# Performance work log

Measured on AMD Instinct MI355X. Metric: run time of the kernel, lower is better.

## Reference

```python
import jax, jax.numpy as jnp
import numpy as np

N = 100000
NUM_CLASSES = 10
EPS = 1e-16
NEG_SLOPE = 0.2


def gat_conv(x, src, dst, W, a_src, a_dst, bias, heads, out_ch, concat):
    # x: [N, F_in]; src/dst: [E] (message flows src -> dst, PyG convention)
    n = x.shape[0]
    h = (x @ W).reshape(n, heads, out_ch)              # [N, H, C]
    al = jnp.sum(h * a_src, axis=-1)                   # [N, H] source attention term
    ar = jnp.sum(h * a_dst, axis=-1)                   # [N, H] target attention term
    e = jax.nn.leaky_relu(al[src] + ar[dst], NEG_SLOPE)  # [E, H]
    # segment softmax over incoming edges of each dst node
    m = jax.ops.segment_max(e, dst, num_segments=n)    # [N, H]
    ex = jnp.exp(e - m[dst])                           # [E, H]
    denom = jax.ops.segment_sum(ex, dst, num_segments=n)  # [N, H]
    alpha = ex / (denom[dst] + EPS)                    # [E, H]
    msg = h[src] * alpha[..., None]                    # [E, H, C]
    out = jax.ops.segment_sum(msg, dst, num_segments=n)   # [N, H, C]
    out = out.reshape(n, heads * out_ch) if concat else out.mean(axis=1)
    return out + bias


def setup_inputs() -> dict:
    key = jax.random.key(0)
    ks = jax.random.split(key, 10)
    F_in, H1, C1 = 512, 8, 8
    x = jax.random.normal(ks[0], (N, F_in), dtype=jnp.float32)
    edge_index = jax.random.randint(ks[1], (2, 1600000), 0, N, dtype=jnp.int64)
    s = 0.05
    return {
        "x": x,
        "edge_index": edge_index,
        "W1": jax.random.normal(ks[2], (F_in, H1 * C1), dtype=jnp.float32) * s,
        "a_src1": jax.random.normal(ks[3], (H1, C1), dtype=jnp.float32) * s,
        "a_dst1": jax.random.normal(ks[4], (H1, C1), dtype=jnp.float32) * s,
        "b1": jnp.zeros((H1 * C1,), dtype=jnp.float32),
        "W2": jax.random.normal(ks[5], (H1 * C1, NUM_CLASSES), dtype=jnp.float32) * s,
        "a_src2": jax.random.normal(ks[6], (1, NUM_CLASSES), dtype=jnp.float32) * s,
        "a_dst2": jax.random.normal(ks[7], (1, NUM_CLASSES), dtype=jnp.float32) * s,
        "b2": jnp.zeros((NUM_CLASSES,), dtype=jnp.float32),
    }


def reference(x, edge_index, W1, a_src1, a_dst1, b1, W2, a_src2, a_dst2, b2):
    # add self-loops (GATConv default add_self_loops=True)
    loops = jnp.arange(N, dtype=edge_index.dtype)
    src = jnp.concatenate([edge_index[0], loops])
    dst = jnp.concatenate([edge_index[1], loops])
    # eval mode: dropout(p=0.6) is identity
    h = gat_conv(x, src, dst, W1, a_src1, a_dst1, b1, heads=8, out_ch=8, concat=True)
    h = jax.nn.elu(h)
    out = gat_conv(h, src, dst, W2, a_src2, a_dst2, b2, heads=1, out_ch=NUM_CLASSES, concat=True)
    return jax.nn.log_softmax(out, axis=1)
```

## Files before the change

kernel.cpp:

```cpp
#include <hip/hip_runtime.h>
#include <math.h>

#define NN 100000
#define NEDGE 1600000
#define NTOT 1700000
#define FIN 512
#define NH1 8
#define NC1 8
#define F1 64
#define NC2 10
#define SLOPE 0.2f
#define EPSF 1e-16f
#define SCAN_BLK 1024
#define NB ((NN + SCAN_BLK - 1) / SCAN_BLK)

__device__ __forceinline__ float lrelu(float x) { return x > 0.f ? x : SLOPE * x; }
__device__ __forceinline__ float eluf(float x) { return x > 0.f ? x : __expf(x) - 1.f; }

__device__ __forceinline__ unsigned short f2bf_rne(float f) {
    unsigned int u = __float_as_uint(f);
    unsigned int r = (u + 0x7FFFu + ((u >> 16) & 1u)) >> 16;
    return (unsigned short)r;
}
__device__ __forceinline__ float bf2f(unsigned short b) {
    return __uint_as_float(((unsigned int)b) << 16);
}

#define GBM 256
#define GBK 32
#define AS_STRIDE 260

__global__ __launch_bounds__(256) void k_gemm1(const float* __restrict__ x,
                                               const float* __restrict__ W,
                                               const float* __restrict__ asrc,
                                               const float* __restrict__ adst,
                                               unsigned short* __restrict__ h1b,
                                               float* __restrict__ al,
                                               float* __restrict__ ar)
{
    __shared__ float As[GBK][AS_STRIDE];
    __shared__ float Bs[GBK][F1];
    __shared__ float sas[F1], sad[F1];
    const int tid = threadIdx.x;
    const int row0 = blockIdx.x * GBM;
    const int ti = tid >> 3;
    const int tj = tid & 7;
    const int ti8 = ti << 3, tj8 = tj << 3;
    if (tid < F1) { sas[tid] = asrc[tid]; sad[tid] = adst[tid]; }
    float acc[8][8] = {};

    for (int k0 = 0; k0 < FIN; k0 += GBK) {
        #pragma unroll
        for (int l = 0; l < 8; ++l) {
            int idx = tid + l * 256;
            int r = idx >> 3, c4 = idx & 7;
            int gr = row0 + r;
            float4 v = make_float4(0.f, 0.f, 0.f, 0.f);
            if (gr < NN) v = *(const float4*)(x + (size_t)gr * FIN + k0 + (c4 << 2));
            As[(c4 << 2) + 0][r] = v.x;
            As[(c4 << 2) + 1][r] = v.y;
            As[(c4 << 2) + 2][r] = v.z;
            As[(c4 << 2) + 3][r] = v.w;
        }
        #pragma unroll
        for (int l = 0; l < 2; ++l) {
            int idx = tid + l * 256;
            int r = idx >> 4, c4 = idx & 15;
            *(float4*)&Bs[r][c4 << 2] = *(const float4*)(W + (size_t)(k0 + r) * F1 + (c4 << 2));
        }
        __syncthreads();
        #pragma unroll
        for (int kk = 0; kk < GBK; ++kk) {
            float4 a0 = *(const float4*)&As[kk][ti8];
            float4 a1 = *(const float4*)&As[kk][ti8 + 4];
            float4 b0 = *(const float4*)&Bs[kk][tj8];
            float4 b1 = *(const float4*)&Bs[kk][tj8 + 4];
            float a[8] = {a0.x, a0.y, a0.z, a0.w, a1.x, a1.y, a1.z, a1.w};
            float b[8] = {b0.x, b0.y, b0.z, b0.w, b1.x, b1.y, b1.z, b1.w};
            #pragma unroll
            for (int i = 0; i < 8; ++i)
                #pragma unroll
                for (int j = 0; j < 8; ++j)
                    acc[i][j] += a[i] * b[j];
        }
        __syncthreads();
    }
    #pragma unroll
    for (int i = 0; i < 8; ++i) {
        int gr = row0 + ti8 + i;
        if (gr >= NN) break;
        float av = 0.f, dv = 0.f;
        unsigned short u[8];
        #pragma unroll
        for (int c = 0; c < 8; ++c) {
            av += acc[i][c] * sas[tj8 + c];
            dv += acc[i][c] * sad[tj8 + c];
            u[c] = f2bf_rne(acc[i][c]);
        }
        al[gr * NH1 + tj] = av;
        ar[gr * NH1 + tj] = dv;
        *(uint4*)(h1b + (size_t)gr * F1 + tj8) = *(uint4*)u;
    }
}

__global__ void k_init1(int* __restrict__ cnt)
{
    int i = blockIdx.x * blockDim.x + threadIdx.x;
    if (i < NN) cnt[i] = 1;
}

__global__ void k_hist(const int* __restrict__ ei, int* __restrict__ cnt,
                       int* __restrict__ pos)
{
    int e = blockIdx.x * blockDim.x + threadIdx.x;
    if (e >= NEDGE) return;
    pos[e] = atomicAdd(&cnt[ei[NEDGE + e]], 1);
}

__global__ __launch_bounds__(256) void k_scan1(const int* __restrict__ cnt,
                                               int* __restrict__ off,
                                               int* __restrict__ bsum)
{
    __shared__ int s[256];
    int t = threadIdx.x;
    int base = blockIdx.x * SCAN_BLK + t * 4;
    int c0 = (base + 0 < NN) ? cnt[base + 0] : 0;
    int c1 = (base + 1 < NN) ? cnt[base + 1] : 0;
    int c2 = (base + 2 < NN) ? cnt[base + 2] : 0;
    int c3 = (base + 3 < NN) ? cnt[base + 3] : 0;
    int ts = c0 + c1 + c2 + c3;
    s[t] = ts;
    __syncthreads();
    #pragma unroll
    for (int d = 1; d < 256; d <<= 1) {
        int v = (t >= d) ? s[t - d] : 0;
        __syncthreads();
        s[t] += v;
        __syncthreads();
    }
    int run = s[t] - ts;
    if (t == 255) bsum[blockIdx.x] = s[255];
    if (base + 0 < NN) off[base + 0] = run; run += c0;
    if (base + 1 < NN) off[base + 1] = run; run += c1;
    if (base + 2 < NN) off[base + 2] = run; run += c2;
    if (base + 3 < NN) off[base + 3] = run;
}

__global__ void k_scan2(int* __restrict__ bsum, int* __restrict__ off)
{
    __shared__ int s[128];
    int t = threadIdx.x;
    int v = (t < NB) ? bsum[t] : 0;
    s[t] = v;
    __syncthreads();
    #pragma unroll
    for (int d = 1; d < 128; d <<= 1) {
        int w = (t >= d) ? s[t - d] : 0;
        __syncthreads();
        s[t] += w;
        __syncthreads();
    }
    if (t < NB) bsum[t] = s[t] - v;
    if (t == 0) off[NN] = NTOT;
}

__global__ void k_scan3(int* __restrict__ off, const int* __restrict__ bsum,
                        int* __restrict__ esrc)
{
    int i = blockIdx.x * blockDim.x + threadIdx.x;
    if (i >= NN) return;
    int o = off[i] + bsum[i >> 10];
    off[i] = o;
    esrc[o] = i;
}

__global__ void k_scatter(const int* __restrict__ ei, const int* __restrict__ off,
                          const int* __restrict__ pos, int* __restrict__ esrc)
{
    int e = blockIdx.x * blockDim.x + threadIdx.x;
    if (e >= NEDGE) return;
    esrc[off[ei[NEDGE + e]] + pos[e]] = ei[e];
}

__global__ __launch_bounds__(256) void k_agg1csr(const int* __restrict__ off,
                                                 const int* __restrict__ esrc,
                                                 const float* __restrict__ al,
                                                 const float* __restrict__ ar,
                                                 const unsigned short* __restrict__ h1b,
                                                 const float* __restrict__ b1,
                                                 float* __restrict__ g)
{
    int node = blockIdx.x * 4 + (threadIdx.x >> 6);
    int lane = threadIdx.x & 63;
    int h = lane >> 3;
    int beg = off[node], end = off[node + 1];
    float arn = ar[node * NH1 + h];
    float acc0 = 0.f, acc1 = 0.f, ds0 = 0.f, ds1 = 0.f;
    int i = beg;
    for (; i + 1 < end; i += 2) {
        int s0 = esrc[i], s1 = esrc[i + 1];
        float e0 = __expf(lrelu(al[s0 * NH1 + h] + arn));
        float e1 = __expf(lrelu(al[s1 * NH1 + h] + arn));
        acc0 += bf2f(h1b[(size_t)s0 * F1 + lane]) * e0; ds0 += e0;
        acc1 += bf2f(h1b[(size_t)s1 * F1 + lane]) * e1; ds1 += e1;
    }
    if (i < end) {
        int s0 = esrc[i];
        float e0 = __expf(lrelu(al[s0 * NH1 + h] + arn));
        acc0 += bf2f(h1b[(size_t)s0 * F1 + lane]) * e0; ds0 += e0;
    }
    float v = (acc0 + acc1) / (ds0 + ds1 + EPSF);
    g[(size_t)node * F1 + lane] = eluf(v + b1[lane]);
}

__global__ __launch_bounds__(256) void k_l2prep(
    const float* __restrict__ g, const float* __restrict__ W2,
    const float* __restrict__ asrc2, const float* __restrict__ adst2,
    float* __restrict__ h2, float* __restrict__ al2, float* __restrict__ ar2)
{
    __shared__ float sW[F1 * NC2];
    __shared__ float sas[NC2], sad[NC2];
    int tid = threadIdx.x;
    for (int i = tid; i < F1 * NC2; i += 256) sW[i] = W2[i];
    if (tid < NC2) { sas[tid] = asrc2[tid]; sad[tid] = adst2[tid]; }
    __syncthreads();
    int n = blockIdx.x * 256 + tid;
    if (n >= NN) return;

    const float* row = g + (size_t)n * F1;
    float acc[NC2] = {};
    #pragma unroll
    for (int c = 0; c < F1; c += 4) {
        float4 v = *(const float4*)(row + c);
        #pragma unroll
        for (int o = 0; o < NC2; ++o) {
            acc[o] += v.x * sW[(c + 0) * NC2 + o] + v.y * sW[(c + 1) * NC2 + o]
                    + v.z * sW[(c + 2) * NC2 + o] + v.w * sW[(c + 3) * NC2 + o];
        }
    }
    float sa = 0.f, sd = 0.f;
    #pragma unroll
    for (int o = 0; o < NC2; ++o) { sa += acc[o] * sas[o]; sd += acc[o] * sad[o]; }
    al2[n] = sa; ar2[n] = sd;
    float* h2p = h2 + (size_t)n * NC2;
    #pragma unroll
    for (int o = 0; o < NC2; ++o) h2p[o] = acc[o];
}

__global__ __launch_bounds__(256) void k_agg2csr(const int* __restrict__ off,
                                                 const int* __restrict__ esrc,
                                                 const float* __restrict__ al2,
                                                 const float* __restrict__ ar2,
                                                 const float* __restrict__ h2,
                                                 const float* __restrict__ b2,
                                                 float* __restrict__ out)
{
    int node = blockIdx.x * 16 + (threadIdx.x >> 4);
    int li = threadIdx.x & 15;
    int beg = off[node], end = off[node + 1];
    float arn = ar2[node];
    float acc = 0.f, dsum = 0.f;
    for (int i = beg; i < end; ++i) {
        int s = esrc[i];
        float ev = __expf(lrelu(al2[s] + arn));
        if (li < NC2) acc += h2[(size_t)s * NC2 + li] * ev;
        dsum += ev;
    }
    float z = (li < NC2) ? acc / (dsum + EPSF) + b2[li] : -1e30f;
    float m = z;
    #pragma unroll
    for (int d = 8; d >= 1; d >>= 1) m = fmaxf(m, __shfl_xor(m, d, 16));
    float ex = (li < NC2) ? __expf(z - m) : 0.f;
    float ss = ex;
    #pragma unroll
    for (int d = 8; d >= 1; d >>= 1) ss += __shfl_xor(ss, d, 16);
    float ls = __logf(ss) + m;
    if (li < NC2) out[(size_t)node * NC2 + li] = z - ls;
}

extern "C" void kernel_launch(void* const* d_in, const int* in_sizes, int n_in,
                              void* d_out, int out_size, void* d_ws, size_t ws_size,
                              hipStream_t stream)
{
    const float* x    = (const float*)d_in[0];
    const int*   ei   = (const int*)d_in[1];
    const float* W1   = (const float*)d_in[2];
    const float* as1  = (const float*)d_in[3];
    const float* ad1  = (const float*)d_in[4];
    const float* b1   = (const float*)d_in[5];
    const float* W2   = (const float*)d_in[6];
    const float* as2  = (const float*)d_in[7];
    const float* ad2  = (const float*)d_in[8];
    const float* b2   = (const float*)d_in[9];
    float* out = (float*)d_out;

    char* ws = (char*)d_ws;
    unsigned short* h1b = (unsigned short*)ws;
    float* al1 = (float*)(ws + (size_t)NN * F1 * 2);
    float* ar1 = al1 + (size_t)NN * NH1;
    float* g   = ar1 + (size_t)NN * NH1;
    int* cnt   = (int*)(g + (size_t)NN * F1);
    int* off   = cnt + NN;
    int* bsum  = off + NN + 1;
    int* esrc  = bsum + 128;
    int* pos   = esrc + NTOT;
    float* h2  = (float*)(pos + NEDGE);
    float* al2 = h2 + (size_t)NN * NC2;
    float* ar2 = al2 + NN;

    k_gemm1<<<(NN + GBM - 1) / GBM, 256, 0, stream>>>(x, W1, as1, ad1, h1b, al1, ar1);
    k_init1<<<(NN + 255) / 256, 256, 0, stream>>>(cnt);
    k_hist<<<(NEDGE + 255) / 256, 256, 0, stream>>>(ei, cnt, pos);
    k_scan1<<<NB, 256, 0, stream>>>(cnt, off, bsum);
    k_scan2<<<1, 128, 0, stream>>>(bsum, off);
    k_scan3<<<(NN + 255) / 256, 256, 0, stream>>>(off, bsum, esrc);
    k_scatter<<<(NEDGE + 255) / 256, 256, 0, stream>>>(ei, off, pos, esrc);
    k_agg1csr<<<NN / 4, 256, 0, stream>>>(off, esrc, al1, ar1, h1b, b1, g);
    k_l2prep<<<(NN + 255) / 256, 256, 0, stream>>>(g, W2, as2, ad2, h2, al2, ar2);
    k_agg2csr<<<NN / 16, 256, 0, stream>>>(off, esrc, al2, ar2, h2, b2, out);
}
```

Baseline: 679.7 us.

## Use bf16 MFMA for layer-1 GEMM and pack layer-2 node features

Replaces the fp32 FMA tiled GEMM for x@W1 with a bf16 MFMA 16x16x32 kernel, converting x to bf16 on load and pre-transposing W1 to bf16 in a fused init kernel. The attention logits al/ar are moved out of the GEMM epilogue into a separate k_prep1 kernel that reads the bf16 h1. Layer-2 h2, al2 and ar2 are packed into one 12-float record per node so the aggregation gather reads a single contiguous row and broadcasts al2 by shuffle. Risks include extra bf16 rounding of x and W and the added kernel launch; the GEMM uses narrow per-element bf16 stores.

```diff
diff --git a/kernel.cpp b/kernel.cpp
--- a/kernel.cpp
+++ b/kernel.cpp
@@ -14,6 +14,9 @@
 #define SCAN_BLK 1024
 #define NB ((NN + SCAN_BLK - 1) / SCAN_BLK)
 
+typedef short short8 __attribute__((ext_vector_type(8)));
+typedef float f32x4 __attribute__((ext_vector_type(4)));
+
 __device__ __forceinline__ float lrelu(float x) { return x > 0.f ? x : SLOPE * x; }
 __device__ __forceinline__ float eluf(float x) { return x > 0.f ? x : __expf(x) - 1.f; }
 
@@ -26,87 +29,88 @@
     return __uint_as_float(((unsigned int)b) << 16);
 }
 
-#define GBM 256
-#define GBK 32
-#define AS_STRIDE 260
+__global__ void k_init(const float* __restrict__ W, unsigned short* __restrict__ wT,
+                       int* __restrict__ cnt)
+{
+    int i = blockIdx.x * 256 + threadIdx.x;
+    if (i < NN) cnt[i] = 1;
+    if (i < F1 * FIN) {
+        int n = i & 63, k = i >> 6;
+        wT[n * FIN + k] = f2bf_rne(W[k * F1 + n]);
+    }
+}
+
+#define LDA 40
 
 __global__ __launch_bounds__(256) void k_gemm1(const float* __restrict__ x,
-                                               const float* __restrict__ W,
-                                               const float* __restrict__ asrc,
-                                               const float* __restrict__ adst,
-                                               unsigned short* __restrict__ h1b,
-                                               float* __restrict__ al,
-                                               float* __restrict__ ar)
-{
-    __shared__ float As[GBK][AS_STRIDE];
-    __shared__ float Bs[GBK][F1];
-    __shared__ float sas[F1], sad[F1];
+                                               const unsigned short* __restrict__ wT,
+                                               unsigned short* __restrict__ h1b)
+{
+    __shared__ unsigned short Al[64][LDA];
+    __shared__ unsigned short Bl[64][LDA];
     const int tid = threadIdx.x;
-    const int row0 = blockIdx.x * GBM;
-    const int ti = tid >> 3;
-    const int tj = tid & 7;
-    const int ti8 = ti << 3, tj8 = tj << 3;
-    if (tid < F1) { sas[tid] = asrc[tid]; sad[tid] = adst[tid]; }
-    float acc[8][8] = {};
-
-    for (int k0 = 0; k0 < FIN; k0 += GBK) {
+    const int row0 = blockIdx.x * 64;
+    const int w  = tid >> 6;
+    const int l  = tid & 63;
+    const int lr = l & 15;
+    const int lg = l >> 4;
+    f32x4 acc[4] = {};
+
+    for (int k0 = 0; k0 < FIN; k0 += 32) {
         #pragma unroll
-        for (int l = 0; l < 8; ++l) {
-            int idx = tid + l * 256;
-            int r = idx >> 3, c4 = idx & 7;
+        for (int t2 = 0; t2 < 2; ++t2) {
+            int idx = tid + t2 * 256;
+            int r = idx >> 3, q = idx & 7;
             int gr = row0 + r;
-            float4 v = make_float4(0.f, 0.f, 0.f, 0.f);
-            if (gr < NN) v = *(const float4*)(x + (size_t)gr * FIN + k0 + (c4 << 2));
-            As[(c4 << 2) + 0][r] = v.x;
-            As[(c4 << 2) + 1][r] = v.y;
-            As[(c4 << 2) + 2][r] = v.z;
-            As[(c4 << 2) + 3][r] = v.w;
-        }
+            float4 v = (gr < NN) ? *(const float4*)(x + (size_t)gr * FIN + k0 + 4 * q)
+                                 : make_float4(0.f, 0.f, 0.f, 0.f);
+            ushort4 u;
+            u.x = f2bf_rne(v.x); u.y = f2bf_rne(v.y);
+            u.z = f2bf_rne(v.z); u.w = f2bf_rne(v.w);
+            *(ushort4*)&Al[r][4 * q] = u;
+        }
+        {
+            int n = tid >> 2, q = tid & 3;
+            *(uint4*)&Bl[n][8 * q] = *(const uint4*)(wT + (size_t)n * FIN + k0 + 8 * q);
+        }
+        __syncthreads();
+        short8 a = *(const short8*)&Al[16 * w + lr][8 * lg];
         #pragma unroll
-        for (int l = 0; l < 2; ++l) {
-            int idx = tid + l * 256;
-            int r = idx >> 4, c4 = idx & 15;
-            *(float4*)&Bs[r][c4 << 2] = *(const float4*)(W + (size_t)(k0 + r) * F1 + (c4 << 2));
-        }
-        __syncthreads();
-        #pragma unroll
-        for (int kk = 0; kk < GBK; ++kk) {
-            float4 a0 = *(const float4*)&As[kk][ti8];
-            float4 a1 = *(const float4*)&As[kk][ti8 + 4];
-            float4 b0 = *(const float4*)&Bs[kk][tj8];
-            float4 b1 = *(const float4*)&Bs[kk][tj8 + 4];
-            float a[8] = {a0.x, a0.y, a0.z, a0.w, a1.x, a1.y, a1.z, a1.w};
-            float b[8] = {b0.x, b0.y, b0.z, b0.w, b1.x, b1.y, b1.z, b1.w};
+        for (int nt = 0; nt < 4; ++nt) {
+            short8 b = *(const short8*)&Bl[16 * nt + lr][8 * lg];
+            acc[nt] = __builtin_amdgcn_mfma_f32_16x16x32_bf16(a, b, acc[nt], 0, 0, 0);
+        }
+        __syncthreads();
+    }
+    #pragma unroll
+    for (int r = 0; r < 4; ++r) {
+        int gr = row0 + 16 * w + 4 * lg + r;
+        if (gr < NN) {
             #pragma unroll
-            for (int i = 0; i < 8; ++i)
-                #pragma unroll
-                for (int j = 0; j < 8; ++j)
-                    acc[i][j] += a[i] * b[j];
-        }
-        __syncthreads();
-    }
-    #pragma unroll
-    for (int i = 0; i < 8; ++i) {
-        int gr = row0 + ti8 + i;
-        if (gr >= NN) break;
-        float av = 0.f, dv = 0.f;
-        unsigned short u[8];
-        #pragma unroll
-        for (int c = 0; c < 8; ++c) {
-            av += acc[i][c] * sas[tj8 + c];
-            dv += acc[i][c] * sad[tj8 + c];
-            u[c] = f2bf_rne(acc[i][c]);
-        }
-        al[gr * NH1 + tj] = av;
-        ar[gr * NH1 + tj] = dv;
-        *(uint4*)(h1b + (size_t)gr * F1 + tj8) = *(uint4*)u;
-    }
-}
-
-__global__ void k_init1(int* __restrict__ cnt)
+            for (int nt = 0; nt < 4; ++nt)
+                h1b[(size_t)gr * F1 + 16 * nt + lr] = f2bf_rne(acc[nt][r]);
+        }
+    }
+}
+
+__global__ void k_prep1(const unsigned short* __restrict__ h1b,
+                        const float* __restrict__ asrc, const float* __restrict__ adst,
+                        float* __restrict__ al, float* __restrict__ ar)
 {
     int i = blockIdx.x * blockDim.x + threadIdx.x;
-    if (i < NN) cnt[i] = 1;
+    if (i >= NN * NH1) return;
+    int node = i >> 3, hh = i & 7;
+    const unsigned short* hp = h1b + (size_t)node * F1 + hh * NC1;
+    ushort4 u0 = *(const ushort4*)hp;
+    ushort4 u1 = *(const ushort4*)(hp + 4);
+    float hv[8] = {bf2f(u0.x), bf2f(u0.y), bf2f(u0.z), bf2f(u0.w),
+                   bf2f(u1.x), bf2f(u1.y), bf2f(u1.z), bf2f(u1.w)};
+    const float* as = asrc + hh * NC1;
+    const float* ad = adst + hh * NC1;
+    float sa = 0.f, sd = 0.f;
+    #pragma unroll
+    for (int c = 0; c < 8; ++c) { sa += hv[c] * as[c]; sd += hv[c] * ad[c]; }
+    al[i] = sa; ar[i] = sd;
 }
 
 __global__ void k_hist(const int* __restrict__ ei, int* __restrict__ cnt,
@@ -216,7 +220,7 @@
 __global__ __launch_bounds__(256) void k_l2prep(
     const float* __restrict__ g, const float* __restrict__ W2,
     const float* __restrict__ asrc2, const float* __restrict__ adst2,
-    float* __restrict__ h2, float* __restrict__ al2, float* __restrict__ ar2)
+    float* __restrict__ packed)
 {
     __shared__ float sW[F1 * NC2];
     __shared__ float sas[NC2], sad[NC2];
@@ -241,29 +245,29 @@
     float sa = 0.f, sd = 0.f;
     #pragma unroll
     for (int o = 0; o < NC2; ++o) { sa += acc[o] * sas[o]; sd += acc[o] * sad[o]; }
-    al2[n] = sa; ar2[n] = sd;
-    float* h2p = h2 + (size_t)n * NC2;
-    #pragma unroll
-    for (int o = 0; o < NC2; ++o) h2p[o] = acc[o];
+    float* p = packed + (size_t)n * 12;
+    #pragma unroll
+    for (int o = 0; o < NC2; ++o) p[o] = acc[o];
+    p[10] = sa; p[11] = sd;
 }
 
 __global__ __launch_bounds__(256) void k_agg2csr(const int* __restrict__ off,
                                                  const int* __restrict__ esrc,
-                                                 const float* __restrict__ al2,
-                                                 const float* __restrict__ ar2,
-                                                 const float* __restrict__ h2,
+                                                 const float* __restrict__ packed,
                                                  const float* __restrict__ b2,
                                                  float* __restrict__ out)
 {
     int node = blockIdx.x * 16 + (threadIdx.x >> 4);
     int li = threadIdx.x & 15;
     int beg = off[node], end = off[node + 1];
-    float arn = ar2[node];
+    float arn = packed[(size_t)node * 12 + 11];
     float acc = 0.f, dsum = 0.f;
     for (int i = beg; i < end; ++i) {
         int s = esrc[i];
-        float ev = __expf(lrelu(al2[s] + arn));
-        if (li < NC2) acc += h2[(size_t)s * NC2 + li] * ev;
+        float val = (li < 12) ? packed[(size_t)s * 12 + li] : 0.f;
+        float al2s = __shfl(val, 10, 16);
+        float ev = __expf(lrelu(al2s + arn));
+        if (li < NC2) acc += val * ev;
         dsum += ev;
     }
     float z = (li < NC2) ? acc / (dsum + EPSF) + b2[li] : -1e30f;
@@ -296,26 +300,26 @@
 
     char* ws = (char*)d_ws;
     unsigned short* h1b = (unsigned short*)ws;
-    float* al1 = (float*)(ws + (size_t)NN * F1 * 2);
+    unsigned short* wT  = h1b + (size_t)NN * F1;
+    float* al1 = (float*)(wT + (size_t)F1 * FIN);
     float* ar1 = al1 + (size_t)NN * NH1;
     float* g   = ar1 + (size_t)NN * NH1;
-    int* cnt   = (int*)(g + (size_t)NN * F1);
+    float* packed = g + (size_t)NN * F1;
+    int* cnt   = (int*)(packed + (size_t)NN * 12);
     int* off   = cnt + NN;
     int* bsum  = off + NN + 1;
     int* esrc  = bsum + 128;
     int* pos   = esrc + NTOT;
-    float* h2  = (float*)(pos + NEDGE);
-    float* al2 = h2 + (size_t)NN * NC2;
-    float* ar2 = al2 + NN;
-
-    k_gemm1<<<(NN + GBM - 1) / GBM, 256, 0, stream>>>(x, W1, as1, ad1, h1b, al1, ar1);
-    k_init1<<<(NN + 255) / 256, 256, 0, stream>>>(cnt);
+
+    k_init<<<(NN + 255) / 256, 256, 0, stream>>>(W1, wT, cnt);
+    k_gemm1<<<(NN + 63) / 64, 256, 0, stream>>>(x, wT, h1b);
     k_hist<<<(NEDGE + 255) / 256, 256, 0, stream>>>(ei, cnt, pos);
     k_scan1<<<NB, 256, 0, stream>>>(cnt, off, bsum);
     k_scan2<<<1, 128, 0, stream>>>(bsum, off);
     k_scan3<<<(NN + 255) / 256, 256, 0, stream>>>(off, bsum, esrc);
     k_scatter<<<(NEDGE + 255) / 256, 256, 0, stream>>>(ei, off, pos, esrc);
+    k_prep1<<<(NN * NH1 + 255) / 256, 256, 0, stream>>>(h1b, as1, ad1, al1, ar1);
     k_agg1csr<<<NN / 4, 256, 0, stream>>>(off, esrc, al1, ar1, h1b, b1, g);
-    k_l2prep<<<(NN + 255) / 256, 256, 0, stream>>>(g, W2, as2, ad2, h2, al2, ar2);
-    k_agg2csr<<<NN / 16, 256, 0, stream>>>(off, esrc, al2, ar2, h2, b2, out);
-}
+    k_l2prep<<<(NN + 255) / 256, 256, 0, stream>>>(g, W2, as2, ad2, packed);
+    k_agg2csr<<<NN / 16, 256, 0, stream>>>(off, esrc, packed, b2, out);
+}
```

New measurement: 606.5 us. 1.12x faster.
